# Kernel optimization log

Hardware: AMD Instinct MI355X
Metric: run time of the kernel (lower is better)

The kernel has to match this reference:

```python
import jax, jax.numpy as jnp
import numpy as np

N, G, C, H, S = 16384, 100, 10, 32, 10  # batch, nb_genes, nb_chrom, hidden, signature
BN_EPS = 1e-5
SLOPE = 0.2


def setup_inputs() -> dict:
    key = jax.random.key(0)
    k = jax.random.split(key, 7)
    x = jax.random.randint(k[0], (N, G), 0, 3)                      # categorical genotype per gene
    emb = jax.random.normal(k[1], (G, 3, H), dtype=jnp.float32)      # per-gene entity embedding tables
    gene_att = jax.random.normal(k[2], (C, H), dtype=jnp.float32)    # GeneAttentionLayer attention matrix
    chrom_att = jax.random.normal(k[3], (1, H), dtype=jnp.float32)   # ChromAttentionLayer attention vector
    W = jax.random.normal(k[4], (H, S), dtype=jnp.float32) * 0.1     # linear layer weight
    b = jnp.zeros((S,), dtype=jnp.float32)                           # linear layer bias
    bn_gamma = jnp.ones((S,), dtype=jnp.float32)
    bn_beta = jnp.zeros((S,), dtype=jnp.float32)
    return {"x": x, "emb": emb, "gene_att": gene_att, "chrom_att": chrom_att,
            "W": W, "b": b, "bn_gamma": bn_gamma, "bn_beta": bn_beta}


def reference(x, emb, gene_att, chrom_att, W, b, bn_gamma, bn_beta):
    nb_genes, nb_chrom, hid = emb.shape[0], gene_att.shape[0], emb.shape[2]
    genes_per_chrom = nb_genes // nb_chrom
    # chrom composition matrix: comp[i, j] = 1 iff gene j belongs to chromosome i (contiguous blocks)
    comp = (jnp.arange(nb_genes) // genes_per_chrom == jnp.arange(nb_chrom)[:, None]).astype(emb.dtype)

    # --- entity embedding: h[n, g] = emb[g, x[n, g]]  -> (N, G, H)
    h = emb[jnp.arange(nb_genes)[None, :], x]

    # --- GeneAttentionLayer (avoids the dense (N, C, G, H) intermediate of the torch code)
    att = jnp.einsum('ch,ngh->ncg', gene_att, h) * comp[None]        # (N, C, G)
    mask = (att != 0).astype(h.dtype)                                # matches att.bool().byte()
    a = jnp.exp(jax.nn.leaky_relu(att, SLOPE)) * mask
    a = a / jnp.maximum(a.sum(axis=2, keepdims=True), 1e-10)
    chrom = jnp.einsum('ncg,ngh->nch', a, h)                         # (N, C, H) chromosome embeddings
    chrom = jax.nn.relu(chrom)                                       # dropout p=0 -> identity

    # --- ChromAttentionLayer
    catt = jnp.einsum('h,nch->nc', chrom_att[0], chrom)              # (N, C)
    ca = jnp.exp(jax.nn.leaky_relu(catt, SLOPE))
    ca = ca / ca.sum(axis=1, keepdims=True)
    g = jnp.einsum('nc,nch->nh', ca, chrom)                          # (N, H)
    g = jax.nn.relu(g)

    # --- linear + batch norm (training-mode batch statistics, biased variance as in torch BN)
    y = g @ W + b                                                    # (N, S)
    mu = y.mean(axis=0)
    var = ((y - mu) ** 2).mean(axis=0)
    return (y - mu) / jnp.sqrt(var + BN_EPS) * bn_gamma + bn_beta
```

## Files before the change

kernel.cpp:

```cpp
#include <hip/hip_runtime.h>
#include <hip/hip_fp16.h>

#define NROWS 16384
#define NG 100
#define NC 10
#define NH 32
#define NS 10
#define GPC 10
#define SLOPE 0.2f
#define BN_EPS 1e-5f

#define EPADH 36
#define RPB 32
#define BLOCK_A 512
#define NB (NROWS / RPB)

template<int CTRL>
__device__ __forceinline__ float dpp_add(float v) {
    int x = __builtin_bit_cast(int, v);
    int y = __builtin_amdgcn_update_dpp(0, x, CTRL, 0xF, 0xF, true);
    return v + __builtin_bit_cast(float, y);
}
__device__ __forceinline__ float row16_allreduce(float v) {
    v = dpp_add<0x128>(v);
    v = dpp_add<0x124>(v);
    v = dpp_add<0x122>(v);
    v = dpp_add<0x121>(v);
    return v;
}

#define GATHER(c, earr, harr)                                              \
    _Pragma("unroll")                                                      \
    for (int gp = 0; gp < GPC; ++gp) {                                     \
        const int g_ = (c) * GPC + gp;                                     \
        const unsigned xg_ = (pk[g_ >> 4] >> ((g_ & 15) * 2)) & 3u;        \
        const int r3_ = g_ * 3 + (int)xg_;                                 \
        earr[gp] = eL[r3_];                                                \
        harr[gp] = *reinterpret_cast<const unsigned*>(&embL[r3_ * EPADH + o * 2]); \
    }

#define COMPUTE(earr, harr) do {                                           \
    float suma_ = 0.f;                                                     \
    _Pragma("unroll")                                                      \
    for (int gp = 0; gp < GPC; ++gp) suma_ += earr[gp];                    \
    const float inv_ = 1.f / fmaxf(suma_, 1e-10f);                         \
    float2 ch_ = {0.f, 0.f};                                               \
    _Pragma("unroll")                                                      \
    for (int gp = 0; gp < GPC; ++gp) {                                     \
        float2 hf_ = __half22float2(__builtin_bit_cast(__half2, harr[gp]));\
        ch_.x = fmaf(earr[gp], hf_.x, ch_.x);                              \
        ch_.y = fmaf(earr[gp], hf_.y, ch_.y);                              \
    }                                                                      \
    ch_.x = fmaxf(ch_.x, 0.f);    \
    ch_.y = fmaxf(ch_.y, 0.f);                                            \
    float pc_ = ch_.x * ca.x + ch_.y * ca.y;                               \
    pc_ = row16_allreduce(pc_);                      \
    pc_ *= inv_;                                           \
    const float lc_ = pc_ > 0.f ? pc_ : SLOPE * pc_;                       \
    const float ec_ = __expf(lc_);                                         \
    const float w_ = ec_ * inv_;                                          \
    num.x = fmaf(w_, ch_.x, num.x);                                        \
    num.y = fmaf(w_, ch_.y, num.y);                                        \
    den += ec_;                                                            \
} while (0)

template<bool SLOTS>
__global__ __launch_bounds__(BLOCK_A, 4) void gga_main(
    const int* __restrict__ x, const float* __restrict__ emb,
    const float* __restrict__ gene_att, const float* __restrict__ chrom_att,
    const float* __restrict__ W, const float* __restrict__ b,
    float* __restrict__ y, float* __restrict__ P)
{
    __shared__ __half embL[300 * EPADH];
    __shared__ float eL[300];
    __shared__ float WTL[NS * NH];
    __shared__ float bL[NS];
    __shared__ unsigned xpL[RPB * 8];
    __shared__ float sAcc[2 * NS];

    const int t = threadIdx.x;
    const int n0 = blockIdx.x * RPB;

    for (int i = t; i < 2400; i += BLOCK_A) {
        float4 v = reinterpret_cast<const float4*>(emb)[i];
        int f = i << 2;
        int row = f >> 5, h = f & 31;
        __half2 lo = __floats2half2_rn(v.x, v.y);
        __half2 hi = __floats2half2_rn(v.z, v.w);
        uint2 u;
        u.x = __builtin_bit_cast(unsigned, lo);
        u.y = __builtin_bit_cast(unsigned, hi);
        *reinterpret_cast<uint2*>(&embL[row * EPADH + h]) = u;
    }
    for (int i = t; i < NH * NS; i += BLOCK_A) {
        int s = i >> 5, h = i & 31;
        WTL[i] = W[h * NS + s];
    }
    if (t < NS) bL[t] = b[t];
    if (t < 2 * NS) sAcc[t] = 0.f;
    if (t < 300) {
        const int g = t / 3;
        const float* ga = gene_att + (g / GPC) * NH;
        const float* e = emb + t * NH;
        float s = 0.f;
#pragma unroll
        for (int k = 0; k < NH; k += 4) {
            float4 ev = *reinterpret_cast<const float4*>(e + k);
            float4 gv = *reinterpret_cast<const float4*>(ga + k);
            s = fmaf(gv.x, ev.x, s); s = fmaf(gv.y, ev.y, s);
            s = fmaf(gv.z, ev.z, s); s = fmaf(gv.w, ev.w, s);
        }
        const float lk = s > 0.f ? s : SLOPE * s;
        eL[t] = (s != 0.f) ? __expf(lk) : 0.f;
    }
    if (t < 256) {
        const int r = t >> 3, w = t & 7;
        unsigned pw = 0u;
        if (w < 7) {
            const int4* p = reinterpret_cast<const int4*>(x + (n0 + r) * NG + w * 16);
            const int nv = (w < 6) ? 4 : 1;
#pragma unroll
            for (int i = 0; i < 4; ++i) {
                if (i < nv) {
                    int4 v = p[i];
                    pw |= ((unsigned)v.x & 3u) << (i * 8 + 0);
                    pw |= ((unsigned)v.y & 3u) << (i * 8 + 2);
                    pw |= ((unsigned)v.z & 3u) << (i * 8 + 4);
                    pw |= ((unsigned)v.w & 3u) << (i * 8 + 6);
                }
            }
        }
        xpL[r * 8 + w] = pw;
    }
    __syncthreads();

    const int lr = t >> 4;
    const int o = t & 15;
    const int n = n0 + lr;

    const float2 ca = reinterpret_cast<const float2*>(chrom_att)[o];

    const uint4 pa = *reinterpret_cast<const uint4*>(&xpL[lr * 8]);
    const uint4 pb = *reinterpret_cast<const uint4*>(&xpL[lr * 8 + 4]);
    const unsigned pk[8] = {pa.x, pa.y, pa.z, pa.w, pb.x, pb.y, pb.z, pb.w};

    float2 num = {0.f, 0.f};
    float den = 0.f;

    float eA[GPC], eB[GPC];
    unsigned hA[GPC], hB[GPC];
    GATHER(0, eA, hA);
#pragma unroll
    for (int c = 0; c < NC; ++c) {
        if ((c & 1) == 0) {
            if (c + 1 < NC) { GATHER(c + 1, eB, hB); }
            COMPUTE(eA, hA);
        } else {
            if (c + 1 < NC) { GATHER(c + 1, eA, hA); }
            COMPUTE(eB, hB);
        }
    }

    const float invd = 1.f / den;
    const float g0 = fmaxf(num.x * invd, 0.f);
    const float g1 = fmaxf(num.y * invd, 0.f);

    float ys[NS];
#pragma unroll
    for (int s = 0; s < NS; ++s) {
        const float2 wv = *reinterpret_cast<const float2*>(&WTL[s * NH + o * 2]);
        float p = g0 * wv.x + g1 * wv.y;
        p = row16_allreduce(p);
        ys[s] = p + bL[s];
    }

    if (o == 0) {
        float2* yp = reinterpret_cast<float2*>(y + n * NS);
#pragma unroll
        for (int s2 = 0; s2 < 5; ++s2) yp[s2] = make_float2(ys[2 * s2], ys[2 * s2 + 1]);
    }

#pragma unroll
    for (int s = 0; s < NS; ++s) {
        float v = ys[s];
        float v2 = ys[s] * ys[s];
        v += __shfl_xor(v, 16);  v2 += __shfl_xor(v2, 16);
        v += __shfl_xor(v, 32);  v2 += __shfl_xor(v2, 32);
        if ((t & 63) == 0) {
            atomicAdd(&sAcc[s], v);
            atomicAdd(&sAcc[NS + s], v2);
        }
    }
    __syncthreads();
    if (t < 2 * NS) {
        if (SLOTS) P[t * NB + blockIdx.x] = sAcc[t];
        else       atomicAdd(&P[t], sAcc[t]);
    }
}

template<bool SLOTS>
__global__ __launch_bounds__(256) void gga_bn(
    float* __restrict__ out, const float* __restrict__ P,
    const float* __restrict__ gamma, const float* __restrict__ beta)
{
    __shared__ float red[2 * NS * 8];
    __shared__ float scL[NS], shL[NS];
    const int t = threadIdx.x;

    if (SLOTS) {
        if (t < 2 * NS * 8) {
            const int k = t >> 3, c = t & 7;
            const float4* p4 = reinterpret_cast<const float4*>(P + k * NB + c * 64);
            float s = 0.f;
#pragma unroll
            for (int i = 0; i < 16; ++i) {
                float4 v = p4[i];
                s += v.x + v.y + v.z + v.w;
            }
            red[t] = s;
        }
        __syncthreads();
    }
    if (t < NS) {
        float sm, sq;
        if (SLOTS) {
            sm = 0.f; sq = 0.f;
#pragma unroll
            for (int c = 0; c < 8; ++c) {
                sm += red[t * 8 + c];
                sq += red[(NS + t) * 8 + c];
            }
        } else {
            sm = P[t]; sq = P[NS + t];
        }
        const float mu = sm * (1.f / NROWS);
        float var = sq * (1.f / NROWS) - mu * mu;
        var = fmaxf(var, 0.f);
        const float r = rsqrtf(var + BN_EPS);
        scL[t] = gamma[t] * r;
        shL[t] = beta[t] - mu * scL[t];
    }
    __syncthreads();

    const int i4 = (blockIdx.x * 256 + t) * 4;
    float4 v = *reinterpret_cast<const float4*>(out + i4);
    const int s0 = i4 % NS;
    const int s1 = (s0 + 1) % NS, s2 = (s0 + 2) % NS, s3 = (s0 + 3) % NS;
    v.x = fmaf(v.x, scL[s0], shL[s0]);
    v.y = fmaf(v.y, scL[s1], shL[s1]);
    v.z = fmaf(v.z, scL[s2], shL[s2]);
    v.w = fmaf(v.w, scL[s3], shL[s3]);
    *reinterpret_cast<float4*>(out + i4) = v;
}

extern "C" void kernel_launch(void* const* d_in, const int* in_sizes, int n_in,
                              void* d_out, int out_size, void* d_ws, size_t ws_size,
                              hipStream_t stream) {
    const int*   x         = (const int*)d_in[0];
    const float* emb       = (const float*)d_in[1];
    const float* gene_att  = (const float*)d_in[2];
    const float* chrom_att = (const float*)d_in[3];
    const float* W         = (const float*)d_in[4];
    const float* b         = (const float*)d_in[5];
    const float* bn_gamma  = (const float*)d_in[6];
    const float* bn_beta   = (const float*)d_in[7];

    float* y = (float*)d_out;
    float* P = (float*)d_ws;

    if (ws_size >= (size_t)(2 * NS * NB * sizeof(float))) {
        gga_main<true><<<NB, BLOCK_A, 0, stream>>>(
            x, emb, gene_att, chrom_att, W, b, y, P);
        gga_bn<true><<<(NROWS * NS) / (256 * 4), 256, 0, stream>>>(
            y, P, bn_gamma, bn_beta);
    } else {
        hipMemsetAsync(P, 0, 2 * NS * sizeof(float), stream);
        gga_main<false><<<NB, BLOCK_A, 0, stream>>>(
            x, emb, gene_att, chrom_att, W, b, y, P);
        gga_bn<false><<<(NROWS * NS) / (256 * 4), 256, 0, stream>>>(
            y, P, bn_gamma, bn_beta);
    }
}
```

Before: 25.72 us.

## Interleave half embeddings with attention weights in one shared table

Builds a combined LDS table where each (gene,genotype,lane) entry packs the fp16 embedding pair together with the precomputed exp attention weight. The gather then needs one 8-byte LDS load per gene instead of two separate loads. Building this table needs an extra barrier after eL is computed, and the table is larger than the padded half table it replaces, so fewer blocks may fit per CU. Two smaller changes come with it: the weight sum uses a tree of additions, and the cross-row stats reduction uses DPP row_bcast in place of shuffles, with the lane that performs the atomic moved to the last lane.

```diff
diff --git a/kernel.cpp b/kernel.cpp
--- a/kernel.cpp
+++ b/kernel.cpp
@@ -10,7 +10,6 @@
 #define SLOPE 0.2f
 #define BN_EPS 1e-5f
 
-#define EPADH 36
 #define RPB 32
 #define BLOCK_A 512
 #define NB (NROWS / RPB)
@@ -29,36 +28,39 @@
     return v;
 }
 
-#define GATHER(c, earr, harr)                                              \
+#define GATHER(c, arr)                                                     \
     _Pragma("unroll")                                                      \
     for (int gp = 0; gp < GPC; ++gp) {                                     \
         const int g_ = (c) * GPC + gp;                                     \
         const unsigned xg_ = (pk[g_ >> 4] >> ((g_ & 15) * 2)) & 3u;        \
         const int r3_ = g_ * 3 + (int)xg_;                                 \
-        earr[gp] = eL[r3_];                                                \
-        harr[gp] = *reinterpret_cast<const unsigned*>(&embL[r3_ * EPADH + o * 2]); \
-    }
-
-#define COMPUTE(earr, harr) do {                                           \
-    float suma_ = 0.f;                                                     \
+        arr[gp] = cmbL[r3_ * 16 + o];                                      \
+    }
+
+#define COMPUTE(arr) do {                                                  \
+    float e_[GPC];                                                         \
     _Pragma("unroll")                                                      \
-    for (int gp = 0; gp < GPC; ++gp) suma_ += earr[gp];                    \
+    for (int gp = 0; gp < GPC; ++gp)                                       \
+        e_[gp] = __builtin_bit_cast(float, arr[gp].y);                     \
+    const float s01_ = (e_[0] + e_[1]) + (e_[2] + e_[3]);                  \
+    const float s23_ = (e_[4] + e_[5]) + (e_[6] + e_[7]);                  \
+    const float suma_ = (s01_ + s23_) + (e_[8] + e_[9]);                   \
     const float inv_ = 1.f / fmaxf(suma_, 1e-10f);                         \
     float2 ch_ = {0.f, 0.f};                                               \
     _Pragma("unroll")                                                      \
     for (int gp = 0; gp < GPC; ++gp) {                                     \
-        float2 hf_ = __half22float2(__builtin_bit_cast(__half2, harr[gp]));\
-        ch_.x = fmaf(earr[gp], hf_.x, ch_.x);                              \
-        ch_.y = fmaf(earr[gp], hf_.y, ch_.y);                              \
+        float2 hf_ = __half22float2(__builtin_bit_cast(__half2, arr[gp].x));\
+        ch_.x = fmaf(e_[gp], hf_.x, ch_.x);                                \
+        ch_.y = fmaf(e_[gp], hf_.y, ch_.y);                                \
     }                                                                      \
     ch_.x = fmaxf(ch_.x, 0.f);    \
-    ch_.y = fmaxf(ch_.y, 0.f);                                            \
+    ch_.y = fmaxf(ch_.y, 0.f);                                             \
     float pc_ = ch_.x * ca.x + ch_.y * ca.y;                               \
     pc_ = row16_allreduce(pc_);                      \
     pc_ *= inv_;                                           \
     const float lc_ = pc_ > 0.f ? pc_ : SLOPE * pc_;                       \
     const float ec_ = __expf(lc_);                                         \
-    const float w_ = ec_ * inv_;                                          \
+    const float w_ = ec_ * inv_;                                           \
     num.x = fmaf(w_, ch_.x, num.x);                                        \
     num.y = fmaf(w_, ch_.y, num.y);                                        \
     den += ec_;                                                            \
@@ -71,7 +73,7 @@
     const float* __restrict__ W, const float* __restrict__ b,
     float* __restrict__ y, float* __restrict__ P)
 {
-    __shared__ __half embL[300 * EPADH];
+    __shared__ uint2 cmbL[300 * 16];
     __shared__ float eL[300];
     __shared__ float WTL[NS * NH];
     __shared__ float bL[NS];
@@ -81,23 +83,6 @@
     const int t = threadIdx.x;
     const int n0 = blockIdx.x * RPB;
 
-    for (int i = t; i < 2400; i += BLOCK_A) {
-        float4 v = reinterpret_cast<const float4*>(emb)[i];
-        int f = i << 2;
-        int row = f >> 5, h = f & 31;
-        __half2 lo = __floats2half2_rn(v.x, v.y);
-        __half2 hi = __floats2half2_rn(v.z, v.w);
-        uint2 u;
-        u.x = __builtin_bit_cast(unsigned, lo);
-        u.y = __builtin_bit_cast(unsigned, hi);
-        *reinterpret_cast<uint2*>(&embL[row * EPADH + h]) = u;
-    }
-    for (int i = t; i < NH * NS; i += BLOCK_A) {
-        int s = i >> 5, h = i & 31;
-        WTL[i] = W[h * NS + s];
-    }
-    if (t < NS) bL[t] = b[t];
-    if (t < 2 * NS) sAcc[t] = 0.f;
     if (t < 300) {
         const int g = t / 3;
         const float* ga = gene_att + (g / GPC) * NH;
@@ -113,6 +98,9 @@
         const float lk = s > 0.f ? s : SLOPE * s;
         eL[t] = (s != 0.f) ? __expf(lk) : 0.f;
     }
+    if (t < NH * NS) WTL[t] = W[(t & 31) * NS + (t >> 5)];
+    if (t < NS) bL[t] = b[t];
+    if (t < 2 * NS) sAcc[t] = 0.f;
     if (t < 256) {
         const int r = t >> 3, w = t & 7;
         unsigned pw = 0u;
@@ -134,6 +122,20 @@
     }
     __syncthreads();
 
+#pragma unroll
+    for (int i2 = 0; i2 < 10; ++i2) {
+        const int i = t + i2 * BLOCK_A;
+        if (i < 4800) {
+            float2 hv = reinterpret_cast<const float2*>(emb)[i];
+            __half2 h2 = __floats2half2_rn(hv.x, hv.y);
+            uint2 en;
+            en.x = __builtin_bit_cast(unsigned, h2);
+            en.y = __builtin_bit_cast(unsigned, eL[i >> 4]);
+            cmbL[i] = en;
+        }
+    }
+    __syncthreads();
+
     const int lr = t >> 4;
     const int o = t & 15;
     const int n = n0 + lr;
@@ -147,17 +149,16 @@
     float2 num = {0.f, 0.f};
     float den = 0.f;
 
-    float eA[GPC], eB[GPC];
-    unsigned hA[GPC], hB[GPC];
-    GATHER(0, eA, hA);
+    uint2 hA[GPC], hB[GPC];
+    GATHER(0, hA);
 #pragma unroll
     for (int c = 0; c < NC; ++c) {
         if ((c & 1) == 0) {
-            if (c + 1 < NC) { GATHER(c + 1, eB, hB); }
-            COMPUTE(eA, hA);
+            if (c + 1 < NC) { GATHER(c + 1, hB); }
+            COMPUTE(hA);
         } else {
-            if (c + 1 < NC) { GATHER(c + 1, eA, hA); }
-            COMPUTE(eB, hB);
+            if (c + 1 < NC) { GATHER(c + 1, hA); }
+            COMPUTE(hB);
         }
     }
 
@@ -184,9 +185,9 @@
     for (int s = 0; s < NS; ++s) {
         float v = ys[s];
         float v2 = ys[s] * ys[s];
-        v += __shfl_xor(v, 16);  v2 += __shfl_xor(v2, 16);
-        v += __shfl_xor(v, 32);  v2 += __shfl_xor(v2, 32);
-        if ((t & 63) == 0) {
+        v = dpp_add<0x142>(v);  v2 = dpp_add<0x142>(v2);
+        v = dpp_add<0x143>(v);  v2 = dpp_add<0x143>(v2);
+        if ((t & 63) == 63) {
             atomicAdd(&sAcc[s], v);
             atomicAdd(&sAcc[NS + s], v2);
         }
```

Result: faster. 23.29 us (-9.4%).
